# Performance work log

Hardware: AMD Instinct MI355X
Metric: run time of the kernel (lower is better)

The kernel has to match this reference:

```python
import math
import jax, jax.numpy as jnp
import numpy as np

B, L, DIM, H = 2, 2048, 1024, 16
HD = DIM // H  # 64
EPS = 1e-6


def _rms_norm(x):
    # x: [..., d] float32; no learned weight (trainable=False)
    norm = jax.lax.rsqrt(jnp.mean(jnp.square(x), axis=-1, keepdims=True) + EPS)
    return x * norm


def _apply_rotary(x, cos, sin):
    # x: [b, h, l, d]; cos/sin: [1, 1, l, d//2]
    d = x.shape[-1] // 2
    x1, x2 = x[..., :d], x[..., d:]
    y1 = x1 * cos + x2 * sin
    y2 = -x1 * sin + x2 * cos
    return jnp.concatenate([y1, y2], axis=-1)


def setup_inputs() -> dict:
    key = jax.random.key(0)
    ks = jax.random.split(key, 6)
    s = 0.02
    return {
        "x": jax.random.normal(ks[0], (B, L, DIM), dtype=jnp.float32),
        "v_0": jax.random.normal(ks[1], (B, H, L, HD), dtype=jnp.float32),
        "rope_cos": jnp.cos(jax.random.normal(ks[2], (1, 1, L, HD // 2), dtype=jnp.float32)),
        "rope_sin": jnp.sin(jax.random.normal(ks[2], (1, 1, L, HD // 2), dtype=jnp.float32)),
        "qkv_w": jax.random.normal(ks[3], (3 * DIM, DIM), dtype=jnp.float32) * s,
        "proj_w": jax.random.normal(ks[4], (DIM, DIM), dtype=jnp.float32) * s,
        "lambda_param": jnp.full((1,), 0.5, dtype=jnp.float32),
    }


def reference(x, v_0, rope_cos, rope_sin, qkv_w, proj_w, lambda_param):
    b, l, dim = x.shape
    # QKV projection (no bias): [b, l, 3*dim]
    qkv = jnp.einsum('bld,ed->ble', x, qkv_w)
    # rearrange 'b l (k h d) -> k b h l d'
    qkv = qkv.reshape(b, l, 3, H, HD).transpose(2, 0, 3, 1, 4)
    q, k, v = qkv[0], qkv[1], qkv[2]
    # residual-v blend
    lam = lambda_param.reshape(())
    v = lam * v + (1.0 - lam) * v_0
    # RoPE (done in float32, inputs already float32)
    q = _apply_rotary(q, rope_cos, rope_sin)
    k = _apply_rotary(k, rope_cos, rope_sin)
    # dynamic softmax temperature
    ratio = math.sqrt(math.log(l) / math.log(1040.0))
    k = k * ratio
    # QKNorm (RMSNorm over head_dim, no weight)
    q = _rms_norm(q)
    k = _rms_norm(k)
    # scaled dot product attention
    scale = 1.0 / math.sqrt(HD)
    scores = jnp.einsum('bhqd,bhkd->bhqk', q, k) * scale
    attn = jax.nn.softmax(scores, axis=-1)
    out = jnp.einsum('bhqk,bhkd->bhqd', attn, v)
    # 'b h l d -> b l (h d)' then output projection (no bias)
    out = out.transpose(0, 2, 1, 3).reshape(b, l, dim)
    out = jnp.einsum('bld,ed->ble', out, proj_w)
    return (out, v)
```

## Files before the change

### kernel.cpp

```cpp
#include <hip/hip_runtime.h>

typedef _Float16 f16;
typedef _Float16 f16x8 __attribute__((ext_vector_type(8)));
typedef _Float16 f16x4 __attribute__((ext_vector_type(4)));
typedef float f32x4 __attribute__((ext_vector_type(4)));

#define MFMA32(a, b, c) __builtin_amdgcn_mfma_f32_16x16x32_f16((a), (b), (c), 0, 0, 0)
#define MFMA16(a, b, c) __builtin_amdgcn_mfma_f32_16x16x16f16((a), (b), (c), 0, 0, 0)

constexpr int Bs = 2, Ls = 2048, DIM = 1024, NH = 16, HD = 64;
constexpr int BL = Bs * Ls;
constexpr float EPSV = 1e-6f;
constexpr float SCL2 = 0.125f * 1.44269504f;

__device__ __forceinline__ void async16(void* lds, const void* g) {
  __builtin_amdgcn_global_load_lds((const __attribute__((address_space(1))) void*)g,
                                   (__attribute__((address_space(3))) void*)lds, 16, 0, 0);
}

__device__ __forceinline__ int sw32(int r, int q) {
  int p = r >> 1;
  return p * 64 + ((((r & 1) * 4 + q) ^ (p & 7)) * 8);
}

__global__ void cvt_all_kernel(const float* __restrict__ x, const float* __restrict__ wq,
                               const float* __restrict__ wp, f16* __restrict__ xf,
                               f16* __restrict__ wqf, f16* __restrict__ wpf) {
  constexpr int NX4 = BL * DIM / 4;
  constexpr int NW4 = 3 * DIM * DIM / 4;
  int i = blockIdx.x * blockDim.x + threadIdx.x;
  const float4* src;
  f16x4* dst;
  int j;
  if (i < NX4) {
    src = (const float4*)x; dst = (f16x4*)xf; j = i;
  } else if (i < NX4 + NW4) {
    src = (const float4*)wq; dst = (f16x4*)wqf; j = i - NX4;
  } else {
    src = (const float4*)wp; dst = (f16x4*)wpf; j = i - NX4 - NW4;
  }
  float4 a = src[j];
  f16x4 o = {(f16)a.x, (f16)a.y, (f16)a.z, (f16)a.w};
  dst[j] = o;
}

__global__ __launch_bounds__(256) void qkv_gemm_kernel(
    const f16* __restrict__ A, const f16* __restrict__ W,
    const float* __restrict__ v0,
    const float* __restrict__ rcos, const float* __restrict__ rsin,
    const float* __restrict__ lamp,
    f16* __restrict__ qb, f16* __restrict__ kb, f16* __restrict__ vbT,
    float* __restrict__ vout) {
  constexpr int K = DIM;
  __shared__ alignas(16) f16 sA[128 * 32];
  __shared__ alignas(16) f16 sB[128 * 32];
  const int tid = threadIdx.x;
  const int w = tid >> 6, lane = tid & 63, ln = lane & 15, quad = lane >> 4;
  const int wm = w >> 1, wn = w & 1;
  const int m0 = blockIdx.y * 128, n0 = blockIdx.x * 128;

  const f16* gA[2];
  const f16* gB[2];
#pragma unroll
  for (int s = 0; s < 2; ++s) {
    int lc = tid + s * 256;
    int p = lc >> 3, g = (lc & 7) ^ (p & 7);
    int r = 2 * p + (g >> 2), ce = (g & 3) * 8;
    gA[s] = A + (size_t)(m0 + r) * K + ce;
    gB[s] = W + (size_t)(n0 + r) * K + ce;
  }

  f32x4 acc[4][4] = {};

  for (int it = 0; it < 32; ++it) {
    const int k0 = it * 32;
#pragma unroll
    for (int s = 0; s < 2; ++s) {
      async16(&sA[(tid + s * 256) * 8], gA[s] + k0);
      async16(&sB[(tid + s * 256) * 8], gB[s] + k0);
    }
    __syncthreads();
    f16x8 a[4];
#pragma unroll
    for (int mi = 0; mi < 4; ++mi)
      a[mi] = *(const f16x8*)&sA[sw32(wm * 64 + mi * 16 + ln, quad)];
#pragma unroll
    for (int ni = 0; ni < 4; ++ni) {
      f16x8 b = *(const f16x8*)&sB[sw32(wn * 64 + ni * 16 + ln, quad)];
#pragma unroll
      for (int mi = 0; mi < 4; ++mi) acc[mi][ni] = MFMA32(a[mi], b, acc[mi][ni]);
    }
    __syncthreads();
  }

  const int nb = n0 + wn * 64;
  const int nsec = nb >> 10;
  const int h = (nb & 1023) >> 6;

  if (nsec == 2) {
    const float lam = lamp[0];
#pragma unroll
    for (int mi = 0; mi < 4; ++mi) {
#pragma unroll
      for (int rg = 0; rg < 4; ++rg) {
        int row = m0 + wm * 64 + mi * 16 + quad * 4 + rg;
        int b = row >> 11, l = row & 2047;
        size_t base = ((size_t)(b * NH + h) * Ls + l) * HD;
        int key = l & 63;
        int sidx = ((key >> 2) & 3) * 16 + (key >> 4) * 4 + (key & 3);
        size_t tb = ((size_t)(b * NH + h) * HD) * Ls + (l & ~63) + sidx;
#pragma unroll
        for (int ni = 0; ni < 4; ++ni) {
          int d = ni * 16 + ln;
          float vnew = lam * acc[mi][ni][rg] + (1.0f - lam) * v0[base + d];
          vout[base + d] = vnew;
          vbT[tb + (size_t)d * Ls] = (f16)vnew;
        }
      }
    }
  } else {
    f16* dst = nsec ? kb : qb;
    const float ratio = sqrtf(logf(2048.0f) / logf(1040.0f));
    const float post = nsec ? 1.0f : SCL2;
#pragma unroll
    for (int mi = 0; mi < 4; ++mi) {
#pragma unroll
      for (int rg = 0; rg < 4; ++rg) {
        int row = m0 + wm * 64 + mi * 16 + quad * 4 + rg;
        int b = row >> 11, l = row & 2047;
        float vals[4];
#pragma unroll
        for (int ni = 0; ni < 4; ++ni) vals[ni] = acc[mi][ni][rg];
#pragma unroll
        for (int t = 0; t < 2; ++t) {
          int j = t * 16 + ln;
          float c = rcos[l * 32 + j], s = rsin[l * 32 + j];
          float x1 = vals[t], x2 = vals[t + 2];
          vals[t] = x1 * c + x2 * s;
          vals[t + 2] = -x1 * s + x2 * c;
        }
        if (nsec) {
#pragma unroll
          for (int ni = 0; ni < 4; ++ni) vals[ni] *= ratio;
        }
        float ms = vals[0] * vals[0] + vals[1] * vals[1] + vals[2] * vals[2] + vals[3] * vals[3];
        ms += __shfl_xor(ms, 1);
        ms += __shfl_xor(ms, 2);
        ms += __shfl_xor(ms, 4);
        ms += __shfl_xor(ms, 8);
        float rn = rsqrtf(ms * (1.0f / 64.0f) + EPSV) * post;
        size_t base = ((size_t)(b * NH + h) * Ls + l) * HD;
#pragma unroll
        for (int ni = 0; ni < 4; ++ni) dst[base + ni * 16 + ln] = (f16)(vals[ni] * rn);
      }
    }
  }
}

__global__ __launch_bounds__(256) void flash_kernel(
    const f16* __restrict__ qg, const f16* __restrict__ kg, const f16* __restrict__ vtg,
    f16* __restrict__ ao) {
  __shared__ alignas(16) f16 sK[2][64 * 64];
  __shared__ alignas(16) f16 sVT[2][64 * 64];
  const int tid = threadIdx.x;
  const int w = tid >> 6, lane = tid & 63, ln = lane & 15, quad = lane >> 4;
  const int bx = blockIdx.x;
  const int qt = bx & 15, h = (bx >> 4) & 15, b = bx >> 8;
  const f16* Qh = qg + (size_t)(b * NH + h) * Ls * HD;
  const f16* Kh = kg + (size_t)(b * NH + h) * Ls * HD;
  const f16* VTh = vtg + (size_t)(b * NH + h) * HD * Ls;
  const int q0 = qt * 128;

  f16x8 aq[2][2];
#pragma unroll
  for (int st = 0; st < 2; ++st)
#pragma unroll
    for (int kk = 0; kk < 2; ++kk)
      aq[st][kk] = *(const f16x8*)&Qh[(size_t)(q0 + w * 32 + st * 16 + ln) * HD + kk * 32 + quad * 8];

  f16x8 kr[2], vr[2];
  auto loadKV = [&](int k0) {
#pragma unroll
    for (int s = 0; s < 2; ++s) {
      int ch = tid + s * 256, r = ch >> 3, cg = (ch & 7) * 8;
      kr[s] = *(const f16x8*)&Kh[(size_t)(k0 + r) * HD + cg];
      vr[s] = *(const f16x8*)&VTh[(size_t)r * Ls + k0 + cg];
    }
  };
  auto stageKV = [&](int buf) {
#pragma unroll
    for (int s = 0; s < 2; ++s) {
      int ch = tid + s * 256, r = ch >> 3;
      int po = r * 64 + (((ch & 7) ^ (r & 7)) * 8);
      *(f16x8*)&sK[buf][po] = kr[s];
      *(f16x8*)&sVT[buf][po] = vr[s];
    }
  };

  f32x4 O[2][4] = {};
  float rsum[2] = {0.f, 0.f};

  loadKV(0);
  stageKV(0);
  __syncthreads();

  for (int kt = 0; kt < 32; ++kt) {
    const int cur = kt & 1;
    if (kt < 31) loadKV((kt + 1) * 64);

    f16x4 pf[2][4];
#pragma unroll
    for (int nt = 0; nt < 4; ++nt) {
      int r = nt * 16 + ln;
      f16x8 kf0 = *(const f16x8*)&sK[cur][r * 64 + ((quad ^ (r & 7)) * 8)];
      f16x8 kf1 = *(const f16x8*)&sK[cur][r * 64 + (((4 + quad) ^ (r & 7)) * 8)];
#pragma unroll
      for (int st = 0; st < 2; ++st) {
        f32x4 z = {};
        z = MFMA32(kf0, aq[st][0], z);
        z = MFMA32(kf1, aq[st][1], z);
        float p0 = exp2f(z[0]);
        float p1 = exp2f(z[1]);
        float p2 = exp2f(z[2]);
        float p3 = exp2f(z[3]);
        rsum[st] += (p0 + p1) + (p2 + p3);
        f16x4 pk = {(f16)p0, (f16)p1, (f16)p2, (f16)p3};
        pf[st][nt] = pk;
      }
    }

#pragma unroll
    for (int dt = 0; dt < 4; ++dt) {
      int row = dt * 16 + ln;
#pragma unroll
      for (int nt2 = 0; nt2 < 2; ++nt2) {
        f16x8 vf = *(const f16x8*)&sVT[cur][row * 64 + (((quad * 2 + nt2) ^ (row & 7)) * 8)];
        f16x4 vlo = {vf[0], vf[1], vf[2], vf[3]};
        f16x4 vhi = {vf[4], vf[5], vf[6], vf[7]};
#pragma unroll
        for (int st = 0; st < 2; ++st) {
          O[st][dt] = MFMA16(pf[st][2 * nt2], vlo, O[st][dt]);
          O[st][dt] = MFMA16(pf[st][2 * nt2 + 1], vhi, O[st][dt]);
        }
      }
    }

    if (kt < 31) stageKV(cur ^ 1);
    __syncthreads();
  }

#pragma unroll
  for (int st = 0; st < 2; ++st) {
    float rs = rsum[st];
    rs += __shfl_xor(rs, 16);
    rs += __shfl_xor(rs, 32);
#pragma unroll
    for (int rg = 0; rg < 4; ++rg) {
      float inv = 1.0f / __shfl(rs, quad * 4 + rg);
      int q = q0 + w * 32 + st * 16 + quad * 4 + rg;
      size_t orow = ((size_t)b * Ls + q) * DIM + h * HD;
#pragma unroll
      for (int dt = 0; dt < 4; ++dt)
        ao[orow + dt * 16 + ln] = (f16)(O[st][dt][rg] * inv);
    }
  }
}

__global__ __launch_bounds__(256) void proj_gemm_kernel(
    const f16* __restrict__ A, const f16* __restrict__ W, float* __restrict__ out) {
  constexpr int K = DIM;
  __shared__ alignas(16) f16 sA[64 * 32];
  __shared__ alignas(16) f16 sB[128 * 32];
  const int tid = threadIdx.x;
  const int w = tid >> 6, lane = tid & 63, ln = lane & 15, quad = lane >> 4;
  const int wm = w >> 1, wn = w & 1;
  const int m0 = blockIdx.y * 64, n0 = blockIdx.x * 128;

  const f16* gA;
  {
    int p = tid >> 3, g = (tid & 7) ^ (p & 7);
    gA = A + (size_t)(m0 + 2 * p + (g >> 2)) * K + (g & 3) * 8;
  }
  const f16* gB[2];
#pragma unroll
  for (int s = 0; s < 2; ++s) {
    int lc = tid + s * 256;
    int p = lc >> 3, g = (lc & 7) ^ (p & 7);
    gB[s] = W + (size_t)(n0 + 2 * p + (g >> 2)) * K + (g & 3) * 8;
  }

  f32x4 acc[2][4] = {};

  for (int it = 0; it < 32; ++it) {
    const int k0 = it * 32;
    async16(&sA[tid * 8], gA + k0);
#pragma unroll
    for (int s = 0; s < 2; ++s) async16(&sB[(tid + s * 256) * 8], gB[s] + k0);
    __syncthreads();
    f16x8 a[2];
#pragma unroll
    for (int mi = 0; mi < 2; ++mi)
      a[mi] = *(const f16x8*)&sA[sw32(wm * 32 + mi * 16 + ln, quad)];
#pragma unroll
    for (int ni = 0; ni < 4; ++ni) {
      f16x8 b = *(const f16x8*)&sB[sw32(wn * 64 + ni * 16 + ln, quad)];
#pragma unroll
      for (int mi = 0; mi < 2; ++mi) acc[mi][ni] = MFMA32(a[mi], b, acc[mi][ni]);
    }
    __syncthreads();
  }

#pragma unroll
  for (int mi = 0; mi < 2; ++mi) {
#pragma unroll
    for (int rg = 0; rg < 4; ++rg) {
      int row = m0 + wm * 32 + mi * 16 + quad * 4 + rg;
      size_t o = (size_t)row * DIM + n0 + wn * 64;
#pragma unroll
      for (int ni = 0; ni < 4; ++ni) out[o + ni * 16 + ln] = acc[mi][ni][rg];
    }
  }
}

extern "C" void kernel_launch(void* const* d_in, const int* in_sizes, int n_in,
                              void* d_out, int out_size, void* d_ws, size_t ws_size,
                              hipStream_t stream) {
  (void)in_sizes; (void)n_in; (void)out_size; (void)ws_size;
  const float* x = (const float*)d_in[0];
  const float* v0 = (const float*)d_in[1];
  const float* rcos = (const float*)d_in[2];
  const float* rsin = (const float*)d_in[3];
  const float* wqkv = (const float*)d_in[4];
  const float* wproj = (const float*)d_in[5];
  const float* lamp = (const float*)d_in[6];
  float* out = (float*)d_out;
  float* vout = out + (size_t)BL * DIM;

  char* p = (char*)d_ws;
  auto take = [&](size_t n) { char* q = p; p += ((n + 255) / 256) * 256; return q; };
  f16* xf = (f16*)take((size_t)BL * DIM * 2);
  f16* wqf = (f16*)take((size_t)3 * DIM * DIM * 2);
  f16* wpf = (f16*)take((size_t)DIM * DIM * 2);
  f16* qb = (f16*)take((size_t)BL * DIM * 2);
  f16* kb = (f16*)take((size_t)BL * DIM * 2);
  f16* vbT = (f16*)take((size_t)BL * DIM * 2);
  f16* ao = xf;

  constexpr int NCVT4 = (BL * DIM + 3 * DIM * DIM + DIM * DIM) / 4;
  cvt_all_kernel<<<dim3(NCVT4 / 256), dim3(256), 0, stream>>>(x, wqkv, wproj, xf, wqf, wpf);

  qkv_gemm_kernel<<<dim3(3 * DIM / 128, BL / 128), dim3(256), 0, stream>>>(
      xf, wqf, v0, rcos, rsin, lamp, qb, kb, vbT, vout);

  flash_kernel<<<dim3(Bs * NH * (Ls / 128)), dim3(256), 0, stream>>>(qb, kb, vbT, ao);

  proj_gemm_kernel<<<dim3(DIM / 128, BL / 64), dim3(256), 0, stream>>>(ao, wpf, out);
}
```

Baseline: 241.5 us.

## Split flash attention KV range across two wave groups and use 16x16x32 MFMA for PV

After: 224.2 us. 7.2% less time.

```diff
diff --git a/kernel.cpp b/kernel.cpp
--- a/kernel.cpp
+++ b/kernel.cpp
@@ -6,7 +6,6 @@
 typedef float f32x4 __attribute__((ext_vector_type(4)));
 
 #define MFMA32(a, b, c) __builtin_amdgcn_mfma_f32_16x16x32_f16((a), (b), (c), 0, 0, 0)
-#define MFMA16(a, b, c) __builtin_amdgcn_mfma_f32_16x16x16f16((a), (b), (c), 0, 0, 0)
 
 constexpr int Bs = 2, Ls = 2048, DIM = 1024, NH = 16, HD = 64;
 constexpr int BL = Bs * Ls;
@@ -157,15 +156,18 @@
   }
 }
 
-__global__ __launch_bounds__(256) void flash_kernel(
+__global__ __launch_bounds__(512, 4) void flash_kernel(
     const f16* __restrict__ qg, const f16* __restrict__ kg, const f16* __restrict__ vtg,
     f16* __restrict__ ao) {
-  __shared__ alignas(16) f16 sK[2][64 * 64];
-  __shared__ alignas(16) f16 sVT[2][64 * 64];
+  __shared__ alignas(16) f16 sK[2][2][64 * 64];
+  __shared__ alignas(16) f16 sVT[2][2][64 * 64];
   const int tid = threadIdx.x;
   const int w = tid >> 6, lane = tid & 63, ln = lane & 15, quad = lane >> 4;
+  const int grp = w >> 2, wl = w & 3;
+  const int gt = tid & 255;
   const int bx = blockIdx.x;
-  const int qt = bx & 15, h = (bx >> 4) & 15, b = bx >> 8;
+  const int bh = bx & 31, qt = bx >> 5;
+  const int h = bh & 15, b = bh >> 4;
   const f16* Qh = qg + (size_t)(b * NH + h) * Ls * HD;
   const f16* Kh = kg + (size_t)(b * NH + h) * Ls * HD;
   const f16* VTh = vtg + (size_t)(b * NH + h) * HD * Ls;
@@ -176,13 +178,13 @@
   for (int st = 0; st < 2; ++st)
 #pragma unroll
     for (int kk = 0; kk < 2; ++kk)
-      aq[st][kk] = *(const f16x8*)&Qh[(size_t)(q0 + w * 32 + st * 16 + ln) * HD + kk * 32 + quad * 8];
+      aq[st][kk] = *(const f16x8*)&Qh[(size_t)(q0 + wl * 32 + st * 16 + ln) * HD + kk * 32 + quad * 8];
 
   f16x8 kr[2], vr[2];
   auto loadKV = [&](int k0) {
 #pragma unroll
     for (int s = 0; s < 2; ++s) {
-      int ch = tid + s * 256, r = ch >> 3, cg = (ch & 7) * 8;
+      int ch = gt + s * 256, r = ch >> 3, cg = (ch & 7) * 8;
       kr[s] = *(const f16x8*)&Kh[(size_t)(k0 + r) * HD + cg];
       vr[s] = *(const f16x8*)&VTh[(size_t)r * Ls + k0 + cg];
     }
@@ -190,78 +192,94 @@
   auto stageKV = [&](int buf) {
 #pragma unroll
     for (int s = 0; s < 2; ++s) {
-      int ch = tid + s * 256, r = ch >> 3;
+      int ch = gt + s * 256, r = ch >> 3;
       int po = r * 64 + (((ch & 7) ^ (r & 7)) * 8);
-      *(f16x8*)&sK[buf][po] = kr[s];
-      *(f16x8*)&sVT[buf][po] = vr[s];
+      *(f16x8*)&sK[grp][buf][po] = kr[s];
+      *(f16x8*)&sVT[grp][buf][po] = vr[s];
     }
   };
 
   f32x4 O[2][4] = {};
-  float rsum[2] = {0.f, 0.f};
-
-  loadKV(0);
+  f32x4 racc[2] = {};
+  const f16x8 onesv = {(f16)1.f, (f16)1.f, (f16)1.f, (f16)1.f,
+                       (f16)1.f, (f16)1.f, (f16)1.f, (f16)1.f};
+  const f32x4 zc = {};
+
+  const int kbase = grp << 10;
+  loadKV(kbase);
   stageKV(0);
   __syncthreads();
 
-  for (int kt = 0; kt < 32; ++kt) {
-    const int cur = kt & 1;
-    if (kt < 31) loadKV((kt + 1) * 64);
-
-    f16x4 pf[2][4];
+  for (int t = 0; t < 16; ++t) {
+    const int cur = t & 1;
+    if (t < 15) loadKV(kbase + (t + 1) * 64);
+
+    f16x8 pA[2][2];
 #pragma unroll
     for (int nt = 0; nt < 4; ++nt) {
-      int r = nt * 16 + ln;
-      f16x8 kf0 = *(const f16x8*)&sK[cur][r * 64 + ((quad ^ (r & 7)) * 8)];
-      f16x8 kf1 = *(const f16x8*)&sK[cur][r * 64 + (((4 + quad) ^ (r & 7)) * 8)];
+      const int r = nt * 16 + ln;
+      const f16x8 kf0 = *(const f16x8*)&sK[grp][cur][r * 64 + ((quad ^ (r & 7)) * 8)];
+      const f16x8 kf1 = *(const f16x8*)&sK[grp][cur][r * 64 + (((4 + quad) ^ (r & 7)) * 8)];
 #pragma unroll
       for (int st = 0; st < 2; ++st) {
-        f32x4 z = {};
-        z = MFMA32(kf0, aq[st][0], z);
-        z = MFMA32(kf1, aq[st][1], z);
-        float p0 = exp2f(z[0]);
-        float p1 = exp2f(z[1]);
-        float p2 = exp2f(z[2]);
-        float p3 = exp2f(z[3]);
-        rsum[st] += (p0 + p1) + (p2 + p3);
-        f16x4 pk = {(f16)p0, (f16)p1, (f16)p2, (f16)p3};
-        pf[st][nt] = pk;
-      }
-    }
-
+        f32x4 z = MFMA32(kf1, aq[st][1], MFMA32(kf0, aq[st][0], zc));
+#pragma unroll
+        for (int j = 0; j < 4; ++j)
+          pA[st][nt >> 1][(nt & 1) * 4 + j] = (f16)exp2f(z[j]);
+      }
+    }
+
+    __builtin_amdgcn_s_setprio(1);
+#pragma unroll
+    for (int st = 0; st < 2; ++st) {
+      racc[st] = MFMA32(pA[st][0], onesv, racc[st]);
+      racc[st] = MFMA32(pA[st][1], onesv, racc[st]);
+    }
 #pragma unroll
     for (int dt = 0; dt < 4; ++dt) {
-      int row = dt * 16 + ln;
+      const int row = dt * 16 + ln;
 #pragma unroll
       for (int nt2 = 0; nt2 < 2; ++nt2) {
-        f16x8 vf = *(const f16x8*)&sVT[cur][row * 64 + (((quad * 2 + nt2) ^ (row & 7)) * 8)];
-        f16x4 vlo = {vf[0], vf[1], vf[2], vf[3]};
-        f16x4 vhi = {vf[4], vf[5], vf[6], vf[7]};
-#pragma unroll
-        for (int st = 0; st < 2; ++st) {
-          O[st][dt] = MFMA16(pf[st][2 * nt2], vlo, O[st][dt]);
-          O[st][dt] = MFMA16(pf[st][2 * nt2 + 1], vhi, O[st][dt]);
-        }
-      }
-    }
-
-    if (kt < 31) stageKV(cur ^ 1);
-    __syncthreads();
-  }
-
-#pragma unroll
-  for (int st = 0; st < 2; ++st) {
-    float rs = rsum[st];
-    rs += __shfl_xor(rs, 16);
-    rs += __shfl_xor(rs, 32);
-#pragma unroll
-    for (int rg = 0; rg < 4; ++rg) {
-      float inv = 1.0f / __shfl(rs, quad * 4 + rg);
-      int q = q0 + w * 32 + st * 16 + quad * 4 + rg;
-      size_t orow = ((size_t)b * Ls + q) * DIM + h * HD;
-#pragma unroll
-      for (int dt = 0; dt < 4; ++dt)
-        ao[orow + dt * 16 + ln] = (f16)(O[st][dt][rg] * inv);
+        const f16x8 vf = *(const f16x8*)&sVT[grp][cur][row * 64 + (((quad * 2 + nt2) ^ (row & 7)) * 8)];
+#pragma unroll
+        for (int st = 0; st < 2; ++st)
+          O[st][dt] = MFMA32(pA[st][nt2], vf, O[st][dt]);
+      }
+    }
+    __builtin_amdgcn_s_setprio(0);
+
+    if (t < 15) stageKV(cur ^ 1);
+    __syncthreads();
+  }
+
+  float* cO = (float*)&sK[0][0][0];
+  float* cR = (float*)&sVT[0][0][0];
+  if (grp == 1) {
+#pragma unroll
+    for (int st = 0; st < 2; ++st) {
+#pragma unroll
+      for (int rg = 0; rg < 4; ++rg) {
+        const int ql = wl * 32 + st * 16 + quad * 4 + rg;
+#pragma unroll
+        for (int dt = 0; dt < 4; ++dt) cO[ql * 64 + dt * 16 + ln] = O[st][dt][rg];
+        if (ln == 0) cR[ql] = racc[st][rg];
+      }
+    }
+  }
+  __syncthreads();
+  if (grp == 0) {
+#pragma unroll
+    for (int st = 0; st < 2; ++st) {
+#pragma unroll
+      for (int rg = 0; rg < 4; ++rg) {
+        const int ql = wl * 32 + st * 16 + quad * 4 + rg;
+        const float inv = 1.0f / (racc[st][rg] + cR[ql]);
+        const int q = q0 + ql;
+        const size_t orow = ((size_t)b * Ls + q) * DIM + h * HD;
+#pragma unroll
+        for (int dt = 0; dt < 4; ++dt)
+          ao[orow + dt * 16 + ln] = (f16)((O[st][dt][rg] + cO[ql * 64 + dt * 16 + ln]) * inv);
+      }
     }
   }
 }
@@ -352,7 +370,7 @@
   qkv_gemm_kernel<<<dim3(3 * DIM / 128, BL / 128), dim3(256), 0, stream>>>(
       xf, wqf, v0, rcos, rsin, lamp, qb, kb, vbT, vout);
 
-  flash_kernel<<<dim3(Bs * NH * (Ls / 128)), dim3(256), 0, stream>>>(qb, kb, vbT, ao);
+  flash_kernel<<<dim3(Bs * NH * (Ls / 128)), dim3(512), 0, stream>>>(qb, kb, vbT, ao);
 
   proj_gemm_kernel<<<dim3(DIM / 128, BL / 64), dim3(256), 0, stream>>>(ao, wpf, out);
 }
```
